# Performance work log

Measured on AMD Instinct MI355X. Metric: run time of the kernel, lower is better.

The kernel has to match this reference:

```python
import jax, jax.numpy as jnp
import numpy as np

N_BISECT_ITERS = 50  # entmax library default


def entmax_bisect(X, alpha, n_iter=N_BISECT_ITERS):
    """alpha-entmax over last axis via bisection (Peters & Martins 2019).
    Solves for tau s.t. sum(max((alpha-1)X - tau, 0)^(1/(alpha-1))) = 1."""
    am1 = alpha - 1.0
    inv = 1.0 / am1
    Xa = X * am1
    max_val = jnp.max(Xa, axis=-1, keepdims=True)
    d = X.shape[-1]
    tau_lo = max_val - 1.0                                   # _gp(1, alpha) = 1
    tau_hi = max_val - jnp.asarray(1.0 / d, X.dtype) ** am1  # _gp(1/d, alpha)

    def pfun(tau):
        return jnp.maximum(Xa - tau, 0.0) ** inv

    f_lo = jnp.sum(pfun(tau_lo), axis=-1, keepdims=True) - 1.0

    def body(i, carry):
        tau_lo, dm = carry
        dm = dm * 0.5
        tau_m = tau_lo + dm
        f_m = jnp.sum(pfun(tau_m), axis=-1, keepdims=True) - 1.0
        tau_lo = jnp.where(f_m * f_lo >= 0, tau_m, tau_lo)
        return (tau_lo, dm)

    tau_lo, _ = jax.lax.fori_loop(0, n_iter, body, (tau_lo, tau_hi - tau_lo))
    p = pfun(tau_lo)
    return p / jnp.sum(p, axis=-1, keepdims=True)  # ensure_sum_one


def setup_inputs() -> dict:
    master = jax.random.key(0)
    kq, kk, kv = jax.random.split(master, 3)
    B, H, S, D = 4, 16, 2048, 64
    return {
        "query": jax.random.normal(kq, (B, H, S, D), jnp.float32),
        "key": jax.random.normal(kk, (B, H, S, D), jnp.float32),
        "value": jax.random.normal(kv, (B, H, S, D), jnp.float32),
        "alpha": jnp.float32(1.5),  # canonical entmax-1.5
    }


def reference(query, key, value, alpha):
    D = query.shape[-1]
    scale = 1.0 / jnp.sqrt(jnp.asarray(D, query.dtype))
    scores = jnp.einsum('bhqd,bhkd->bhqk', query, key) * scale  # [B,H,S,S]
    p_attn = entmax_bisect(scores, alpha)
    out = jnp.einsum('bhqk,bhkd->bhqd', p_attn, value)
    return (out, p_attn)
```

## Files before the change

kernel.cpp:

```cpp
#include <hip/hip_runtime.h>
#include <math.h>

#define S_LEN 2048
#define HD    64
#define QT    16
#define NT    1024
#define NW    16
#define NTIL  8
#define CAP   512
#define NITER 28
#define NEWT  8

typedef short s8v __attribute__((ext_vector_type(8)));
typedef float f4v __attribute__((ext_vector_type(4)));

template <bool B> struct BoolT { static constexpr bool value = B; };

__device__ __forceinline__ float wave_sum(float v) {
#pragma unroll
    for (int off = 32; off >= 1; off >>= 1)
        v += __shfl_xor(v, off, 64);
    return v;
}

template <int CTRL, int RMASK>
__device__ __forceinline__ float dpp_add_step(float v) {
    int t = __builtin_amdgcn_update_dpp(0, __float_as_int(v), CTRL, RMASK, 0xf, false);
    return v + __int_as_float(t);
}

__device__ __forceinline__ float dpp_row16_max(float v) {
    constexpr int NEG_INF = (int)0xff800000u;
    int t;
    t = __builtin_amdgcn_update_dpp(NEG_INF, __float_as_int(v), 0x111, 0xf, 0xf, false);
    v = fmaxf(v, __int_as_float(t));
    t = __builtin_amdgcn_update_dpp(NEG_INF, __float_as_int(v), 0x112, 0xf, 0xf, false);
    v = fmaxf(v, __int_as_float(t));
    t = __builtin_amdgcn_update_dpp(NEG_INF, __float_as_int(v), 0x114, 0xf, 0xf, false);
    v = fmaxf(v, __int_as_float(t));
    t = __builtin_amdgcn_update_dpp(NEG_INF, __float_as_int(v), 0x118, 0xf, 0xf, false);
    v = fmaxf(v, __int_as_float(t));
    return v;
}

__device__ __forceinline__ unsigned f2bf2(float lo, float hi) {
    unsigned r;
    asm("v_cvt_pk_bf16_f32 %0, %1, %2" : "=v"(r) : "v"(lo), "v"(hi));
    return r;
}

__device__ __forceinline__ s8v pack_bf8(const float4& x, const float4& y, float sc) {
    union { s8v s; unsigned u[4]; } f;
    f.u[0] = f2bf2(x.x * sc, x.y * sc);
    f.u[1] = f2bf2(x.z * sc, x.w * sc);
    f.u[2] = f2bf2(y.x * sc, y.y * sc);
    f.u[3] = f2bf2(y.z * sc, y.w * sc);
    return f.s;
}

template <bool INV2>
__device__ __forceinline__ float pfun_t(float t, float inv) {
    float u = fmaxf(t, 0.0f);
    return INV2 ? u * u : powf(u, inv);
}

template <int NR>
__device__ __forceinline__ float newton_reg(const float* cvrow, int nc, int lane,
                                            float tau0) {
    float c[NR];
#pragma unroll
    for (int j = 0; j < NR; ++j) {
        int i = lane + 64 * j;
        c[j] = (i < nc) ? cvrow[i] : -3.0e38f;
    }
    float tau = tau0;
#pragma unroll
    for (int it = 0; it < NEWT; ++it) {
        float s1 = 0.0f, s2 = 0.0f;
#pragma unroll
        for (int j = 0; j < NR; ++j) {
            float u = fmaxf(c[j] - tau, 0.0f);
            s1 += u;
            s2 = fmaf(u, u, s2);
        }
        s1 = dpp_add_step<0x111, 0xf>(s1);  s2 = dpp_add_step<0x111, 0xf>(s2);
        s1 = dpp_add_step<0x112, 0xf>(s1);  s2 = dpp_add_step<0x112, 0xf>(s2);
        s1 = dpp_add_step<0x114, 0xf>(s1);  s2 = dpp_add_step<0x114, 0xf>(s2);
        s1 = dpp_add_step<0x118, 0xf>(s1);  s2 = dpp_add_step<0x118, 0xf>(s2);
        s1 = dpp_add_step<0x142, 0xa>(s1);  s2 = dpp_add_step<0x142, 0xa>(s2);
        s1 = dpp_add_step<0x143, 0xc>(s1);  s2 = dpp_add_step<0x143, 0xc>(s2);
        const float S1 = __int_as_float(__builtin_amdgcn_readlane(__float_as_int(s1), 63));
        const float S2 = __int_as_float(__builtin_amdgcn_readlane(__float_as_int(s2), 63));
        tau += (S2 - 1.0f) * 0.5f * __builtin_amdgcn_rcpf(fmaxf(S1, 1e-30f));
    }
    return tau;
}

template <int NR, bool INV2>
__device__ __forceinline__ void bisect_reg(const float* cvrow, int nc, int lane,
                                           float tau_lo0, float tau_hi, float inv,
                                           float& tau_out, float& isum_out) {
    float c[NR];
#pragma unroll
    for (int j = 0; j < NR; ++j) {
        int i = lane + 64 * j;
        c[j] = (i < nc) ? cvrow[i] : -3.0e38f;
    }
    float tau = tau_lo0;
    float s0 = 0.0f;
#pragma unroll
    for (int j = 0; j < NR; ++j) s0 += pfun_t<INV2>(c[j] - tau, inv);
    const float f_lo = wave_sum(s0) - 1.0f;
    float dm = tau_hi - tau_lo0;
    for (int it = 0; it < NITER; ++it) {
        dm *= 0.5f;
        float tm = tau + dm;
        float s = 0.0f;
#pragma unroll
        for (int j = 0; j < NR; ++j) s += pfun_t<INV2>(c[j] - tm, inv);
        float fm = wave_sum(s) - 1.0f;
        if (fm * f_lo >= 0.0f) tau = tm;
    }
    float s = 0.0f;
#pragma unroll
    for (int j = 0; j < NR; ++j) s += pfun_t<INV2>(c[j] - tau, inv);
    float ssum = wave_sum(s);
    tau_out = tau;
    isum_out = 1.0f / ssum;
}

__global__ __launch_bounds__(256)
void pack_kv(const float* __restrict__ Kp, const float* __restrict__ Vp,
             s8v* __restrict__ Kb, s8v* __restrict__ Vb, int nK) {
    int idx = blockIdx.x * 256 + threadIdx.x;
    if (idx < nK) {
        const int lane = idx & 63, frag = (idx >> 6) & 1, tile = (idx >> 7) & 127, bh = idx >> 14;
        const int l16 = lane & 15, quad = lane >> 4;
        const float* src = Kp + ((size_t)(bh * S_LEN + tile * 16 + l16)) * HD + frag * 32 + quad * 8;
        float4 a = *(const float4*)src;
        float4 b = *(const float4*)(src + 4);
        Kb[idx] = pack_bf8(a, b, 1.0f);
    } else {
        int v = idx - nK;
        const int lane = v & 63, dt = (v >> 6) & 3, kt32 = (v >> 8) & 63, bh = v >> 14;
        const int l16 = lane & 15, quad = lane >> 4;
        const int base_row = (kt32 >> 2) * 128 + (kt32 & 3) * 4 + quad;
        const float* src = Vp + ((size_t)(bh * S_LEN + base_row)) * HD + dt * 16 + l16;
        float w[8];
#pragma unroll
        for (int j = 0; j < 8; ++j) w[j] = src[(size_t)j * 16 * HD];
        float4 a = {w[0], w[1], w[2], w[3]};
        float4 b = {w[4], w[5], w[6], w[7]};
        Vb[v] = pack_bf8(a, b, 1.0f);
    }
}

template <bool PREK, bool DPV>
__global__ __launch_bounds__(NT)
void entmax_attn(const float* __restrict__ Qp, const float* __restrict__ Kp,
                 const float* __restrict__ Vp, const float* __restrict__ alphap,
                 float* __restrict__ outp, float* __restrict__ pattn,
                 const s8v* __restrict__ Kbf, const s8v* __restrict__ Vbf) {
    constexpr int SM_BIG = DPV ? (NW * 4096)
                               : (QT * CAP * 4 + QT * CAP * 2);
    __shared__ __align__(16) char smem[SM_BIG];
    float          (*candv)[CAP] = (float(*)[CAP])smem;
    unsigned short (*candi)[CAP] = (unsigned short(*)[CAP])(smem + QT * CAP * 4);

    __shared__ int   ncnt[QT];
    __shared__ float rmaxw[QT][NW];
    __shared__ float rmxf[QT];
    __shared__ float taus[QT];
    __shared__ float isums[QT];
    __shared__ float redw[NW];

    const int tid   = threadIdx.x;
    const int wv    = tid >> 6;
    const int lane  = tid & 63;
    const int quad  = lane >> 4;
    const int l16   = lane & 15;
    const int bh    = blockIdx.y;
    const int q0    = blockIdx.x * QT;
    const int wcol0 = wv * (NTIL * 16);

    const float alpha = alphap[0];
    const float am1   = alpha - 1.0f;
    const float inv   = 1.0f / am1;
    const bool  inv2  = (inv == 2.0f);
    const float xscale = (1.0f / sqrtf((float)HD)) * am1;
    const float gp_d   = powf(1.0f / (float)S_LEN, am1);

    if (tid < QT) ncnt[tid] = 0;

    const float* vbase = Vp + (size_t)bh * S_LEN * HD;

    s8v qa0, qa1;
    {
        const float* qp = Qp + ((size_t)bh * S_LEN + q0 + l16) * HD + quad * 8;
        float4 x0 = *(const float4*)qp;
        float4 x1 = *(const float4*)(qp + 4);
        float4 y0 = *(const float4*)(qp + 32);
        float4 y1 = *(const float4*)(qp + 36);
        qa0 = pack_bf8(x0, x1, xscale);
        qa1 = pack_bf8(y0, y1, xscale);
    }

    f4v xa[NTIL];
    if constexpr (PREK) {
        const s8v* kf = Kbf + ((size_t)bh * (S_LEN / 16) + (wcol0 >> 4)) * 2 * 64 + lane;
        __builtin_amdgcn_s_setprio(1);
#pragma unroll
        for (int t = 0; t < NTIL; ++t) {
            s8v kb0 = kf[(2 * t    ) * 64];
            s8v kb1 = kf[(2 * t + 1) * 64];
            f4v acc = {0.0f, 0.0f, 0.0f, 0.0f};
            acc = __builtin_amdgcn_mfma_f32_16x16x32_bf16(qa0, kb0, acc, 0, 0, 0);
            acc = __builtin_amdgcn_mfma_f32_16x16x32_bf16(qa1, kb1, acc, 0, 0, 0);
            xa[t] = acc;
        }
        __builtin_amdgcn_s_setprio(0);
    } else {
        const float* kbase = Kp + (size_t)bh * S_LEN * HD;
#pragma unroll
        for (int t = 0; t < NTIL; ++t) {
            const float* kp = kbase + ((size_t)(wcol0 + t * 16 + l16)) * HD + quad * 8;
            float4 k0 = *(const float4*)kp;
            float4 k1 = *(const float4*)(kp + 4);
            s8v kb0 = pack_bf8(k0, k1, 1.0f);
            f4v acc = {0.0f, 0.0f, 0.0f, 0.0f};
            acc = __builtin_amdgcn_mfma_f32_16x16x32_bf16(qa0, kb0, acc, 0, 0, 0);
            float4 k2 = *(const float4*)(kp + 32);
            float4 k3 = *(const float4*)(kp + 36);
            s8v kb1 = pack_bf8(k2, k3, 1.0f);
            acc = __builtin_amdgcn_mfma_f32_16x16x32_bf16(qa1, kb1, acc, 0, 0, 0);
            xa[t] = acc;
        }
    }

#pragma unroll
    for (int g = 0; g < 4; ++g) {
        float pm = xa[0][g];
#pragma unroll
        for (int t = 1; t < NTIL; ++t) pm = fmaxf(pm, xa[t][g]);
        pm = dpp_row16_max(pm);
        if (l16 == 15) rmaxw[quad * 4 + g][wv] = pm;
    }
    __syncthreads();
    if (tid < QT) {
        float m = rmaxw[tid][0];
#pragma unroll
        for (int w = 1; w < NW; ++w) m = fmaxf(m, rmaxw[tid][w]);
        rmxf[tid] = m;
    }
    __syncthreads();

#pragma unroll
    for (int g = 0; g < 4; ++g) {
        const int   row = quad * 4 + g;
        const float thr = rmxf[row] - 1.0f;
        unsigned long long bm[NTIL];
        unsigned tq0 = 0, tq1 = 0, tq2 = 0, tq3 = 0;
#pragma unroll
        for (int t = 0; t < NTIL; ++t) {
            bm[t] = __ballot(xa[t][g] > thr);
            tq0 += (unsigned)__popcll(bm[t] & 0x000000000000FFFFull);
            tq1 += (unsigned)__popcll(bm[t] & 0x00000000FFFF0000ull);
            tq2 += (unsigned)__popcll(bm[t] & 0x0000FFFF00000000ull);
            tq3 += (unsigned)__popcll(bm[t] >> 48);
        }
        const int total = (quad & 2) ? ((quad & 1) ? (int)tq3 : (int)tq2)
                                     : ((quad & 1) ? (int)tq1 : (int)tq0);
        int base = 0;
        if (l16 == 0 && total) base = atomicAdd(&ncnt[row], total);
        {
            const int b0 = __builtin_amdgcn_readlane(base, 0);
            const int b1 = __builtin_amdgcn_readlane(base, 16);
            const int b2 = __builtin_amdgcn_readlane(base, 32);
            const int b3 = __builtin_amdgcn_readlane(base, 48);
            base = (quad & 2) ? ((quad & 1) ? b3 : b2)
                              : ((quad & 1) ? b1 : b0);
        }
#pragma unroll
        for (int t = 0; t < NTIL; ++t) {
            const float v = xa[t][g];
            const bool pred = (v > thr);
            unsigned gm16 = (unsigned)((bm[t] >> (quad * 16)) & 0xFFFFull);
            if (pred) {
                int pos = base + __popc(gm16 & ((1u << l16) - 1u));
                if (pos < CAP) {
                    candv[row][pos] = v;
                    if constexpr (!DPV) candi[row][pos] = (unsigned short)(wcol0 + t * 16 + l16);
                }
            }
            base += __popc(gm16);
        }
    }
    __syncthreads();

    auto tail = [&](auto inv2c) {
        constexpr bool INV2 = decltype(inv2c)::value;

        {
            const int row = wv;
            const int nc = ncnt[row];
            if (nc <= CAP) {
                if constexpr (!DPV) {
                    const int ncp = (nc + 7) & ~7;
                    for (int i = nc + lane; i < ncp; i += 64) {
                        candv[row][i] = -3.0e38f;
                        candi[row][i] = 0;
                    }
                }
                const float mx  = rmxf[row];
                const float tl0 = mx - 1.0f;
                const float th  = mx - gp_d;
                float tau, isum;
                if constexpr (INV2) {
                    if (nc <= 256) tau = newton_reg<4>(&candv[row][0], nc, lane, tl0);
                    else           tau = newton_reg<8>(&candv[row][0], nc, lane, tl0);
                    isum = 1.0f;
                } else {
                    if (nc <= 256) bisect_reg<4, INV2>(&candv[row][0], nc, lane, tl0, th, inv, tau, isum);
                    else           bisect_reg<8, INV2>(&candv[row][0], nc, lane, tl0, th, inv, tau, isum);
                }
                if (lane == 0) { taus[row] = tau; isums[row] = isum; }
            }
        }

#pragma unroll 1
        for (int r = 0; r < QT; ++r) {
            if (ncnt[r] > CAP) {
                const float mx = rmxf[r];
                const int g = r & 3;
                const bool mine = (quad == (r >> 2));
                float tau = mx - 1.0f;
                float s0 = 0.0f;
                if (mine) {
#pragma unroll
                    for (int t = 0; t < NTIL; ++t) s0 += pfun_t<INV2>(xa[t][g] - tau, inv);
                }
                s0 = wave_sum(s0);
                if (lane == 0) redw[wv] = s0;
                __syncthreads();
                float f_lo = -1.0f;
                for (int w = 0; w < NW; ++w) f_lo += redw[w];
                __syncthreads();
                float dm = (mx - gp_d) - tau;
                for (int it = 0; it < NITER; ++it) {
                    dm *= 0.5f;
                    float tm = tau + dm;
                    float s = 0.0f;
                    if (mine) {
#pragma unroll
                        for (int t = 0; t < NTIL; ++t) s += pfun_t<INV2>(xa[t][g] - tm, inv);
                    }
                    s = wave_sum(s);
                    if (lane == 0) redw[wv] = s;
                    __syncthreads();
                    float fm = -1.0f;
                    for (int w = 0; w < NW; ++w) fm += redw[w];
                    __syncthreads();
                    if (fm * f_lo >= 0.0f) tau = tm;
                }
                float s = 0.0f;
                if (mine) {
#pragma unroll
                    for (int t = 0; t < NTIL; ++t) s += pfun_t<INV2>(xa[t][g] - tau, inv);
                }
                s = wave_sum(s);
                if (lane == 0) redw[wv] = s;
                __syncthreads();
                float ssum = 0.0f;
                for (int w = 0; w < NW; ++w) ssum += redw[w];
                __syncthreads();
                if (tid == 0) { taus[r] = tau; isums[r] = 1.0f / ssum; }
            }
        }
        __syncthreads();

        if constexpr (DPV) {
            unsigned short* pwf = (unsigned short*)smem + wv * 2048;
            const size_t prow_base = ((size_t)bh * S_LEN + q0) * S_LEN;
#pragma unroll
            for (int g = 0; g < 4; ++g) {
                const int row = quad * 4 + g;
                const float tau  = taus[row];
                const float isum = isums[row];
                float* prow = pattn + prow_base + (size_t)row * S_LEN + wcol0 + l16;
                union { s8v s; unsigned u[4]; } pk;
                float pprev = 0.0f;
#pragma unroll
                for (int t = 0; t < NTIL; ++t) {
                    float p2 = pfun_t<INV2>(xa[t][g] - tau, inv);
                    __builtin_nontemporal_store(p2 * isum, &prow[t * 16]);
                    if (t & 1) pk.u[t >> 1] = f2bf2(pprev, p2);
                    else       pprev = p2;
                }
                const int c = (l16 ^ row) & 15;
                *(s8v*)&pwf[row * 128 + c * 8] = pk.s;
            }
            s8v afrag[4];
#pragma unroll
            for (int kt = 0; kt < 4; ++kt) {
                const int c = ((kt * 4 + quad) ^ l16) & 15;
                afrag[kt] = *(const s8v*)&pwf[l16 * 128 + c * 8];
            }
            const s8v* vf = Vbf + ((size_t)bh * (S_LEN / 32) + (wcol0 >> 5)) * 4 * 64 + lane;
            f4v oacc[4];
#pragma unroll
            for (int dt = 0; dt < 4; ++dt) oacc[dt] = (f4v){0.0f, 0.0f, 0.0f, 0.0f};
            __builtin_amdgcn_s_setprio(1);
#pragma unroll
            for (int kt = 0; kt < 4; ++kt) {
#pragma unroll
                for (int dt = 0; dt < 4; ++dt) {
                    s8v b = vf[(kt * 4 + dt) * 64];
                    oacc[dt] = __builtin_amdgcn_mfma_f32_16x16x32_bf16(afrag[kt], b, oacc[dt], 0, 0, 0);
                }
            }
            __builtin_amdgcn_s_setprio(0);
            float* pr = (float*)pwf;
#pragma unroll
            for (int dt = 0; dt < 4; ++dt) {
#pragma unroll
                for (int g = 0; g < 4; ++g) {
                    pr[(quad * 4 + g) * 64 + ((dt * 16 + l16) ^ (quad << 4))] = oacc[dt][g];
                }
            }
            __syncthreads();
            const int rd = lane ^ ((wv >> 2) << 4);
            float s = 0.0f;
#pragma unroll
            for (int w = 0; w < NW; ++w) s += ((float*)smem)[w * 1024 + wv * 64 + rd];
            __builtin_nontemporal_store(s * isums[wv],
                &outp[((size_t)bh * S_LEN + q0 + wv) * HD + lane]);
        } else {
            const size_t prow_base = ((size_t)bh * S_LEN + q0) * S_LEN;
#pragma unroll
            for (int g = 0; g < 4; ++g) {
                const int row = quad * 4 + g;
                const float tau  = taus[row];
                const float isum = isums[row];
                float* prow = pattn + prow_base + (size_t)row * S_LEN + wcol0 + l16;
#pragma unroll
                for (int t = 0; t < NTIL; ++t) {
                    prow[t * 16] = pfun_t<INV2>(xa[t][g] - tau, inv) * isum;
                }
            }
            __threadfence_block();
            __syncthreads();

            const int row  = wv;
            const int qrow = q0 + row;
            const int nc   = ncnt[row];
            const float tau  = taus[row];
            const float isum = isums[row];
            float oacc = 0.0f;
            if (nc <= CAP) {
                const int ncp = (nc + 7) & ~7;
                for (int i = lane; i < ncp; i += 64)
                    candv[row][i] = pfun_t<INV2>(candv[row][i] - tau, inv);
                float oacc1 = 0.0f;
                for (int i = 0; i < ncp; i += 8) {
#pragma unroll
                    for (int u = 0; u < 8; u += 2) {
                        oacc  = fmaf(candv[row][i + u],
                                     vbase[(size_t)candi[row][i + u] * HD + lane], oacc);
                        oacc1 = fmaf(candv[row][i + u + 1],
                                     vbase[(size_t)candi[row][i + u + 1] * HD + lane], oacc1);
                    }
                }
                oacc = (oacc + oacc1) * isum;
            } else {
                const float* prow = pattn + ((size_t)bh * S_LEN + qrow) * S_LEN;
                for (int k = 0; k < S_LEN; ++k)
                    oacc = fmaf(prow[k], vbase[(size_t)k * HD + lane], oacc);
            }
            outp[((size_t)bh * S_LEN + qrow) * HD + lane] = oacc;
        }
    };

    if (inv2) tail(BoolT<true>{});
    else      tail(BoolT<false>{});
}

extern "C" void kernel_launch(void* const* d_in, const int* in_sizes, int n_in,
                              void* d_out, int out_size, void* d_ws, size_t ws_size,
                              hipStream_t stream) {
    const float* Q = (const float*)d_in[0];
    const float* K = (const float*)d_in[1];
    const float* V = (const float*)d_in[2];
    const float* A = (const float*)d_in[3];
    float* out = (float*)d_out;
    const int BH = in_sizes[0] / (S_LEN * HD);
    float* p = out + (size_t)BH * S_LEN * HD;
    dim3 grid(S_LEN / QT, BH);

    const size_t kb_bytes = (size_t)BH * S_LEN * HD * sizeof(short);
    const int nK = BH * (S_LEN / 16) * 2 * 64;
    const int nV = BH * (S_LEN / 32) * 4 * 64;

    if (d_ws != nullptr && ws_size >= 2 * kb_bytes) {
        s8v* Kb = (s8v*)d_ws;
        s8v* Vb = (s8v*)((char*)d_ws + kb_bytes);
        pack_kv<<<dim3((nK + nV) / 256), 256, 0, stream>>>(K, V, Kb, Vb, nK);
        entmax_attn<true, true><<<grid, NT, 0, stream>>>(Q, K, V, A, out, p, Kb, Vb);
    } else if (d_ws != nullptr && ws_size >= kb_bytes) {
        s8v* Kb = (s8v*)d_ws;
        pack_kv<<<dim3(nK / 256), 256, 0, stream>>>(K, V, Kb, nullptr, nK);
        entmax_attn<true, false><<<grid, NT, 0, stream>>>(Q, K, V, A, out, p, Kb, nullptr);
    } else {
        entmax_attn<false, false><<<grid, NT, 0, stream>>>(Q, K, V, A, out, p, nullptr, nullptr);
    }
}
```

Before: 1.796 ms.

## Halve block size to 8 waves, each wave handling 16 column tiles

Cuts the block from 1024 to 512 threads (8 waves), so each wave covers twice as many key tiles and each tail loop serves two query rows per wave. The candidate compaction, bisection/Newton tail, P·V MFMA accumulation and cross-wave reduction are restructured to loop over two halves. The aim is to shrink cross-wave reduction and barrier cost and raise occupancy via a launch-bounds hint of 4 blocks, at the price of more registers per thread (xa now holds 16 tiles) and more serial work per wave.

```diff
diff --git a/kernel.cpp b/kernel.cpp
--- a/kernel.cpp
+++ b/kernel.cpp
@@ -4,9 +4,9 @@
 #define S_LEN 2048
 #define HD    64
 #define QT    16
-#define NT    1024
-#define NW    16
-#define NTIL  8
+#define NT    512
+#define NW    8
+#define NTIL  16
 #define CAP   512
 #define NITER 28
 #define NEWT  8
@@ -156,12 +156,12 @@
 }
 
 template <bool PREK, bool DPV>
-__global__ __launch_bounds__(NT)
+__global__ __launch_bounds__(NT, 4)
 void entmax_attn(const float* __restrict__ Qp, const float* __restrict__ Kp,
                  const float* __restrict__ Vp, const float* __restrict__ alphap,
                  float* __restrict__ outp, float* __restrict__ pattn,
                  const s8v* __restrict__ Kbf, const s8v* __restrict__ Vbf) {
-    constexpr int SM_BIG = DPV ? (NW * 4096)
+    constexpr int SM_BIG = DPV ? (NW * 4096 > QT * CAP * 4 ? NW * 4096 : QT * CAP * 4)
                                : (QT * CAP * 4 + QT * CAP * 2);
     __shared__ __align__(16) char smem[SM_BIG];
     float          (*candv)[CAP] = (float(*)[CAP])smem;
@@ -255,44 +255,48 @@
     __syncthreads();
 
 #pragma unroll
-    for (int g = 0; g < 4; ++g) {
-        const int   row = quad * 4 + g;
-        const float thr = rmxf[row] - 1.0f;
-        unsigned long long bm[NTIL];
-        unsigned tq0 = 0, tq1 = 0, tq2 = 0, tq3 = 0;
-#pragma unroll
-        for (int t = 0; t < NTIL; ++t) {
-            bm[t] = __ballot(xa[t][g] > thr);
-            tq0 += (unsigned)__popcll(bm[t] & 0x000000000000FFFFull);
-            tq1 += (unsigned)__popcll(bm[t] & 0x00000000FFFF0000ull);
-            tq2 += (unsigned)__popcll(bm[t] & 0x0000FFFF00000000ull);
-            tq3 += (unsigned)__popcll(bm[t] >> 48);
-        }
-        const int total = (quad & 2) ? ((quad & 1) ? (int)tq3 : (int)tq2)
-                                     : ((quad & 1) ? (int)tq1 : (int)tq0);
-        int base = 0;
-        if (l16 == 0 && total) base = atomicAdd(&ncnt[row], total);
-        {
-            const int b0 = __builtin_amdgcn_readlane(base, 0);
-            const int b1 = __builtin_amdgcn_readlane(base, 16);
-            const int b2 = __builtin_amdgcn_readlane(base, 32);
-            const int b3 = __builtin_amdgcn_readlane(base, 48);
-            base = (quad & 2) ? ((quad & 1) ? b3 : b2)
-                              : ((quad & 1) ? b1 : b0);
-        }
-#pragma unroll
-        for (int t = 0; t < NTIL; ++t) {
-            const float v = xa[t][g];
-            const bool pred = (v > thr);
-            unsigned gm16 = (unsigned)((bm[t] >> (quad * 16)) & 0xFFFFull);
-            if (pred) {
-                int pos = base + __popc(gm16 & ((1u << l16) - 1u));
-                if (pos < CAP) {
-                    candv[row][pos] = v;
-                    if constexpr (!DPV) candi[row][pos] = (unsigned short)(wcol0 + t * 16 + l16);
-                }
-            }
-            base += __popc(gm16);
+    for (int h = 0; h < 2; ++h) {
+#pragma unroll
+        for (int g = 0; g < 4; ++g) {
+            const int   row = quad * 4 + g;
+            const float thr = rmxf[row] - 1.0f;
+            unsigned long long bm[8];
+            unsigned tq0 = 0, tq1 = 0, tq2 = 0, tq3 = 0;
+#pragma unroll
+            for (int t = 0; t < 8; ++t) {
+                bm[t] = __ballot(xa[h * 8 + t][g] > thr);
+                tq0 += (unsigned)__popcll(bm[t] & 0x000000000000FFFFull);
+                tq1 += (unsigned)__popcll(bm[t] & 0x00000000FFFF0000ull);
+                tq2 += (unsigned)__popcll(bm[t] & 0x0000FFFF00000000ull);
+                tq3 += (unsigned)__popcll(bm[t] >> 48);
+            }
+            const int total = (quad & 2) ? ((quad & 1) ? (int)tq3 : (int)tq2)
+                                         : ((quad & 1) ? (int)tq1 : (int)tq0);
+            int base = 0;
+            if (l16 == 0 && total) base = atomicAdd(&ncnt[row], total);
+            {
+                const int b0 = __builtin_amdgcn_readlane(base, 0);
+                const int b1 = __builtin_amdgcn_readlane(base, 16);
+                const int b2 = __builtin_amdgcn_readlane(base, 32);
+                const int b3 = __builtin_amdgcn_readlane(base, 48);
+                base = (quad & 2) ? ((quad & 1) ? b3 : b2)
+                                  : ((quad & 1) ? b1 : b0);
+            }
+#pragma unroll
+            for (int t = 0; t < 8; ++t) {
+                const float v = xa[h * 8 + t][g];
+                const bool pred = (v > thr);
+                unsigned gm16 = (unsigned)((bm[t] >> (quad * 16)) & 0xFFFFull);
+                if (pred) {
+                    int pos = base + __popc(gm16 & ((1u << l16) - 1u));
+                    if (pos < CAP) {
+                        candv[row][pos] = v;
+                        if constexpr (!DPV)
+                            candi[row][pos] = (unsigned short)(wcol0 + (h * 8 + t) * 16 + l16);
+                    }
+                }
+                base += __popc(gm16);
+            }
         }
     }
     __syncthreads();
@@ -300,8 +304,9 @@
     auto tail = [&](auto inv2c) {
         constexpr bool INV2 = decltype(inv2c)::value;
 
-        {
-            const int row = wv;
+#pragma unroll 1
+        for (int rr = 0; rr < 2; ++rr) {
+            const int row = wv + rr * NW;
             const int nc = ncnt[row];
             if (nc <= CAP) {
                 if constexpr (!DPV) {
@@ -381,102 +386,112 @@
         if constexpr (DPV) {
             unsigned short* pwf = (unsigned short*)smem + wv * 2048;
             const size_t prow_base = ((size_t)bh * S_LEN + q0) * S_LEN;
+            f4v oacc[4];
+#pragma unroll
+            for (int dt = 0; dt < 4; ++dt) oacc[dt] = (f4v){0.0f, 0.0f, 0.0f, 0.0f};
+#pragma unroll 1
+            for (int h = 0; h < 2; ++h) {
+#pragma unroll
+                for (int g = 0; g < 4; ++g) {
+                    const int row = quad * 4 + g;
+                    const float tau  = taus[row];
+                    const float isum = isums[row];
+                    float* prow = pattn + prow_base + (size_t)row * S_LEN + wcol0 + h * 128 + l16;
+                    union { s8v s; unsigned u[4]; } pk;
+                    float pprev = 0.0f;
+#pragma unroll
+                    for (int t = 0; t < 8; ++t) {
+                        float p2 = pfun_t<INV2>(xa[h * 8 + t][g] - tau, inv);
+                        __builtin_nontemporal_store(p2 * isum, &prow[t * 16]);
+                        if (t & 1) pk.u[t >> 1] = f2bf2(pprev, p2);
+                        else       pprev = p2;
+                    }
+                    const int c = (l16 ^ row) & 15;
+                    *(s8v*)&pwf[row * 128 + c * 8] = pk.s;
+                }
+                s8v afrag[4];
+#pragma unroll
+                for (int kt = 0; kt < 4; ++kt) {
+                    const int c = ((kt * 4 + quad) ^ l16) & 15;
+                    afrag[kt] = *(const s8v*)&pwf[l16 * 128 + c * 8];
+                }
+                const s8v* vf = Vbf + ((size_t)bh * (S_LEN / 32) + wv * 8 + h * 4) * 4 * 64 + lane;
+                __builtin_amdgcn_s_setprio(1);
+#pragma unroll
+                for (int kt = 0; kt < 4; ++kt) {
+#pragma unroll
+                    for (int dt = 0; dt < 4; ++dt) {
+                        s8v b = vf[(kt * 4 + dt) * 64];
+                        oacc[dt] = __builtin_amdgcn_mfma_f32_16x16x32_bf16(afrag[kt], b, oacc[dt], 0, 0, 0);
+                    }
+                }
+                __builtin_amdgcn_s_setprio(0);
+            }
+            float* pr = (float*)pwf;
+#pragma unroll
+            for (int dt = 0; dt < 4; ++dt) {
+#pragma unroll
+                for (int g = 0; g < 4; ++g) {
+                    pr[(quad * 4 + g) * 64 + ((dt * 16 + l16) ^ (quad << 4))] = oacc[dt][g];
+                }
+            }
+            __syncthreads();
+#pragma unroll
+            for (int rr = 0; rr < 2; ++rr) {
+                const int row = wv * 2 + rr;
+                const int rd = lane ^ ((row >> 2) << 4);
+                float s = 0.0f;
+#pragma unroll
+                for (int w = 0; w < NW; ++w) s += ((float*)smem)[w * 1024 + row * 64 + rd];
+                __builtin_nontemporal_store(s * isums[row],
+                    &outp[((size_t)bh * S_LEN + q0 + row) * HD + lane]);
+            }
+        } else {
+            const size_t prow_base = ((size_t)bh * S_LEN + q0) * S_LEN;
 #pragma unroll
             for (int g = 0; g < 4; ++g) {
                 const int row = quad * 4 + g;
                 const float tau  = taus[row];
                 const float isum = isums[row];
                 float* prow = pattn + prow_base + (size_t)row * S_LEN + wcol0 + l16;
-                union { s8v s; unsigned u[4]; } pk;
-                float pprev = 0.0f;
 #pragma unroll
                 for (int t = 0; t < NTIL; ++t) {
-                    float p2 = pfun_t<INV2>(xa[t][g] - tau, inv);
-                    __builtin_nontemporal_store(p2 * isum, &prow[t * 16]);
-                    if (t & 1) pk.u[t >> 1] = f2bf2(pprev, p2);
-                    else       pprev = p2;
-                }
-                const int c = (l16 ^ row) & 15;
-                *(s8v*)&pwf[row * 128 + c * 8] = pk.s;
-            }
-            s8v afrag[4];
-#pragma unroll
-            for (int kt = 0; kt < 4; ++kt) {
-                const int c = ((kt * 4 + quad) ^ l16) & 15;
-                afrag[kt] = *(const s8v*)&pwf[l16 * 128 + c * 8];
-            }
-            const s8v* vf = Vbf + ((size_t)bh * (S_LEN / 32) + (wcol0 >> 5)) * 4 * 64 + lane;
-            f4v oacc[4];
-#pragma unroll
-            for (int dt = 0; dt < 4; ++dt) oacc[dt] = (f4v){0.0f, 0.0f, 0.0f, 0.0f};
-            __builtin_amdgcn_s_setprio(1);
-#pragma unroll
-            for (int kt = 0; kt < 4; ++kt) {
-#pragma unroll
-                for (int dt = 0; dt < 4; ++dt) {
-                    s8v b = vf[(kt * 4 + dt) * 64];
-                    oacc[dt] = __builtin_amdgcn_mfma_f32_16x16x32_bf16(afrag[kt], b, oacc[dt], 0, 0, 0);
-                }
-            }
-            __builtin_amdgcn_s_setprio(0);
-            float* pr = (float*)pwf;
-#pragma unroll
-            for (int dt = 0; dt < 4; ++dt) {
-#pragma unroll
-                for (int g = 0; g < 4; ++g) {
-                    pr[(quad * 4 + g) * 64 + ((dt * 16 + l16) ^ (quad << 4))] = oacc[dt][g];
-                }
-            }
+                    prow[t * 16] = pfun_t<INV2>(xa[t][g] - tau, inv) * isum;
+                }
+            }
+            __threadfence_block();
             __syncthreads();
-            const int rd = lane ^ ((wv >> 2) << 4);
-            float s = 0.0f;
-#pragma unroll
-            for (int w = 0; w < NW; ++w) s += ((float*)smem)[w * 1024 + wv * 64 + rd];
-            __builtin_nontemporal_store(s * isums[wv],
-                &outp[((size_t)bh * S_LEN + q0 + wv) * HD + lane]);
-        } else {
-            const size_t prow_base = ((size_t)bh * S_LEN + q0) * S_LEN;
-#pragma unroll
-            for (int g = 0; g < 4; ++g) {
-                const int row = quad * 4 + g;
+
+#pragma unroll 1
+            for (int rr = 0; rr < 2; ++rr) {
+                const int row  = wv + rr * NW;
+                const int qrow = q0 + row;
+                const int nc   = ncnt[row];
                 const float tau  = taus[row];
                 const float isum = isums[row];
-                float* prow = pattn + prow_base + (size_t)row * S_LEN + wcol0 + l16;
-#pragma unroll
-                for (int t = 0; t < NTIL; ++t) {
-                    prow[t * 16] = pfun_t<INV2>(xa[t][g] - tau, inv) * isum;
-                }
-            }
-            __threadfence_block();
-            __syncthreads();
-
-            const int row  = wv;
-            const int qrow = q0 + row;
-            const int nc   = ncnt[row];
-            const float tau  = taus[row];
-            const float isum = isums[row];
-            float oacc = 0.0f;
-            if (nc <= CAP) {
-                const int ncp = (nc + 7) & ~7;
-                for (int i = lane; i < ncp; i += 64)
-                    candv[row][i] = pfun_t<INV2>(candv[row][i] - tau, inv);
-                float oacc1 = 0.0f;
-                for (int i = 0; i < ncp; i += 8) {
-#pragma unroll
-                    for (int u = 0; u < 8; u += 2) {
-                        oacc  = fmaf(candv[row][i + u],
-                                     vbase[(size_t)candi[row][i + u] * HD + lane], oacc);
-                        oacc1 = fmaf(candv[row][i + u + 1],
-                                     vbase[(size_t)candi[row][i + u + 1] * HD + lane], oacc1);
+                float oacc = 0.0f;
+                if (nc <= CAP) {
+                    const int ncp = (nc + 7) & ~7;
+                    for (int i = lane; i < ncp; i += 64)
+                        candv[row][i] = pfun_t<INV2>(candv[row][i] - tau, inv);
+                    float oacc1 = 0.0f;
+                    for (int i = 0; i < ncp; i += 8) {
+#pragma unroll
+                        for (int u = 0; u < 8; u += 2) {
+                            oacc  = fmaf(candv[row][i + u],
+                                         vbase[(size_t)candi[row][i + u] * HD + lane], oacc);
+                            oacc1 = fmaf(candv[row][i + u + 1],
+                                         vbase[(size_t)candi[row][i + u + 1] * HD + lane], oacc1);
+                        }
                     }
-                }
-                oacc = (oacc + oacc1) * isum;
-            } else {
-                const float* prow = pattn + ((size_t)bh * S_LEN + qrow) * S_LEN;
-                for (int k = 0; k < S_LEN; ++k)
-                    oacc = fmaf(prow[k], vbase[(size_t)k * HD + lane], oacc);
-            }
-            outp[((size_t)bh * S_LEN + qrow) * HD + lane] = oacc;
+                    oacc = (oacc + oacc1) * isum;
+                } else {
+                    const float* prow = pattn + ((size_t)bh * S_LEN + qrow) * S_LEN;
+                    for (int k = 0; k < S_LEN; ++k)
+                        oacc = fmaf(prow[k], vbase[(size_t)k * HD + lane], oacc);
+                }
+                outp[((size_t)bh * S_LEN + qrow) * HD + lane] = oacc;
+            }
         }
     };
 
```

Result: no change. 1.821 ms (+1.4%).
